# Kernel optimization log

Hardware: AMD Instinct MI355X
Metric: run time of the kernel (lower is better)

Reference implementation:

```python
import jax, jax.numpy as jnp
import numpy as np

N_NODES = 100000
N_EDGES = 1600000
D_IN = 64
D_HID = 64
NEG_SLOPE = 0.01  # torch leaky_relu default


def _sage_conv(x, src, dst, W_l, b_l, W_r):
    # PyG SAGEConv (mean aggr): lin_l(mean_j x_j) + lin_r(x_i)
    n = x.shape[0]
    msg = x[src]  # [E, D] irregular gather
    agg = jax.ops.segment_sum(msg, dst, num_segments=n)
    deg = jax.ops.segment_sum(jnp.ones((src.shape[0],), x.dtype), dst, num_segments=n)
    mean = agg / jnp.maximum(deg, 1.0)[:, None]
    return mean @ W_l.T + b_l + x @ W_r.T


def setup_inputs() -> dict:
    key = jax.random.key(0)
    ks = jax.random.split(key, 12)
    x = jax.random.normal(ks[0], (N_NODES, D_IN), dtype=jnp.float32)
    edge_index = jax.random.randint(ks[1], (2, N_EDGES), 0, N_NODES, dtype=jnp.int64)
    s = 1.0 / np.sqrt(D_IN)
    params = {}
    dims = [(D_IN, D_HID), (D_HID, D_HID), (D_HID, D_HID)]
    ki = 2
    for i, (din, dout) in enumerate(dims, start=1):
        sc = 1.0 / np.sqrt(din)
        params[f'W_l{i}'] = jax.random.uniform(ks[ki], (dout, din), minval=-sc, maxval=sc, dtype=jnp.float32); ki += 1
        params[f'b_l{i}'] = jnp.zeros((dout,), jnp.float32)
        params[f'W_r{i}'] = jax.random.uniform(ks[ki], (dout, din), minval=-sc, maxval=sc, dtype=jnp.float32); ki += 1
    sc = 1.0 / np.sqrt(D_HID)
    params['W_out'] = jax.random.uniform(ks[ki], (1, D_HID), minval=-sc, maxval=sc, dtype=jnp.float32)
    params['b_out'] = jnp.zeros((1,), jnp.float32)
    return {'x': x, 'edge_index': edge_index, **params}


def reference(x, edge_index, W_l1, b_l1, W_r1, W_l2, b_l2, W_r2, W_l3, b_l3, W_r3, W_out, b_out):
    src, dst = edge_index[0], edge_index[1]
    h = x
    for (Wl, bl, Wr) in ((W_l1, b_l1, W_r1), (W_l2, b_l2, W_r2), (W_l3, b_l3, W_r3)):
        h = _sage_conv(h, src, dst, Wl, bl, Wr)
        h = jnp.where(h >= 0, h, NEG_SLOPE * h)
        # dropout is identity in eval mode
    return h @ W_out.T + b_out  # [N, 1]
```

## Files before the change

### kernel.cpp

```cpp
#include <hip/hip_runtime.h>
#include <hip/hip_fp16.h>

#define D 64
#define NEG_SLOPE 0.01f
#define CB_SHIFT 9
#define CB_NODES 512
#define MAXCB 256
#define CHUNK 4096
#define BCAP 10240
#define SADJ_CAP 10240
#define SAH 72

typedef _Float16 f16x8 __attribute__((ext_vector_type(8)));
typedef _Float16 f16x4 __attribute__((ext_vector_type(4)));
typedef float    f32x4 __attribute__((ext_vector_type(4)));

struct GemmSmem {
    _Float16 sA[128 * SAH];
    _Float16 sW[2 * 64 * SAH];
};
struct ScatSmem {
    int hist[MAXCB];
    int lofs[MAXCB];
    int gbase[MAXCB];
    int cur[MAXCB];
    int swsum[4];
    unsigned spk[CHUNK];
    unsigned char sbk[CHUNK];
};
union FusedSmem { GemmSmem g; ScatSmem s; };

__device__ __forceinline__ int detect64(const void* __restrict__ ei) {
    int lane = threadIdx.x & 63;
    int v = ((const int*)ei)[2 * lane + 1];
    return (__ballot(v != 0) == 0ULL) ? 1 : 0;
}

__device__ __forceinline__ int edge_at(const void* __restrict__ ei, long long idx, int is64) {
    if (is64) return (int)((const long long*)ei)[idx];
    return ((const int*)ei)[idx];
}

__device__ __forceinline__ void scatter_body(ScatSmem& sm,
        const void* __restrict__ ei, long long E,
        int* __restrict__ bcursor, unsigned* __restrict__ ebuf,
        int ncb, int bid) {
    int t = threadIdx.x;
    sm.hist[t] = 0;
    int is64 = detect64(ei);
    __syncthreads();
    long long start = (long long)bid * CHUNK;
    int ccnt = (int)min((long long)CHUNK, E - start);

    for (int i = t; i < ccnt; i += 256) {
        int d = edge_at(ei, E + start + i, is64);
        atomicAdd(&sm.hist[d >> CB_SHIFT], 1);
    }
    __syncthreads();
    {
        int v = sm.hist[t];
        int lane = t & 63, w = t >> 6;
        int inc = v;
        for (int off = 1; off < 64; off <<= 1) {
            int u = __shfl_up(inc, off, 64);
            if (lane >= off) inc += u;
        }
        if (lane == 63) sm.swsum[w] = inc;
        __syncthreads();
        int wof = 0;
        for (int i = 0; i < w; ++i) wof += sm.swsum[i];
        sm.lofs[t] = wof + inc - v;
    }
    if (t < ncb && sm.hist[t]) sm.gbase[t] = atomicAdd(&bcursor[t], sm.hist[t]);
    __syncthreads();
    sm.cur[t] = sm.lofs[t];
    __syncthreads();

    for (int i = t; i < ccnt; i += 256) {
        int s = edge_at(ei, start + i, is64);
        int d = edge_at(ei, E + start + i, is64);
        int b = d >> CB_SHIFT;
        int slot = atomicAdd(&sm.cur[b], 1);
        sm.spk[slot] = ((unsigned)s << CB_SHIFT) | (unsigned)(d & (CB_NODES - 1));
        sm.sbk[slot] = (unsigned char)b;
    }
    __syncthreads();

    for (int i = t; i < ccnt; i += 256) {
        int b = sm.sbk[i];
        int dst = sm.gbase[b] + (i - sm.lofs[b]);
        if (dst < BCAP) ebuf[(size_t)b * BCAP + dst] = sm.spk[i];
    }
}

__device__ __forceinline__ void gemm_body(GemmSmem& sm,
        const float* __restrict__ h, const float* __restrict__ Wl,
        const float* __restrict__ Wr, const float* __restrict__ bl,
        __half* __restrict__ P, float* __restrict__ R, int N, int bid) {
    int t = threadIdx.x;
    int node_base = bid * 128;

    {
        int r = t >> 1, j = t & 1;
        int gn = node_base + r; if (gn >= N) gn = N - 1;
        const float* src = h + (size_t)gn * D + j * 32;
        _Float16* dst = sm.sA + r * SAH + j * 32;
#pragma unroll
        for (int q = 0; q < 8; ++q) {
            const float4 v = *(const float4*)(src + q * 4);
            f16x4 o = { (_Float16)v.x, (_Float16)v.y, (_Float16)v.z, (_Float16)v.w };
            *(f16x4*)(dst + q * 4) = o;
        }
    }
    {
        const float* W = (t < 128) ? Wl : Wr;
        int tt = t & 127;
        int r = tt >> 1, j = tt & 1;
        const float* src = W + r * D + j * 32;
        _Float16* dst = sm.sW + ((t < 128) ? 0 : 64 * SAH) + r * SAH + j * 32;
#pragma unroll
        for (int q = 0; q < 8; ++q) {
            const float4 v = *(const float4*)(src + q * 4);
            f16x4 o = { (_Float16)v.x, (_Float16)v.y, (_Float16)v.z, (_Float16)v.w };
            *(f16x4*)(dst + q * 4) = o;
        }
    }
    __syncthreads();

    int w = t >> 6, lane = t & 63;
    int lr = lane & 15;
    int lk = lane >> 4;

    f16x8 af[2][2];
#pragma unroll
    for (int mt = 0; mt < 2; ++mt)
#pragma unroll
        for (int ks = 0; ks < 2; ++ks)
            af[mt][ks] = *(const f16x8*)(sm.sA
                + (w * 32 + mt * 16 + lr) * SAH + ks * 32 + lk * 8);

    f32x4 accP[2][4], accR[2][4];
#pragma unroll
    for (int mt = 0; mt < 2; ++mt)
#pragma unroll
        for (int nt = 0; nt < 4; ++nt) {
            accP[mt][nt] = (f32x4){0.f, 0.f, 0.f, 0.f};
            accR[mt][nt] = (f32x4){0.f, 0.f, 0.f, 0.f};
        }

#pragma unroll
    for (int nt = 0; nt < 4; ++nt) {
        const _Float16* wrow = sm.sW + (nt * 16 + lr) * SAH + lk * 8;
        f16x8 b0 = *(const f16x8*)(wrow);
        f16x8 b1 = *(const f16x8*)(wrow + 32);
        f16x8 c0 = *(const f16x8*)(wrow + 64 * SAH);
        f16x8 c1 = *(const f16x8*)(wrow + 64 * SAH + 32);
        accP[0][nt] = __builtin_amdgcn_mfma_f32_16x16x32_f16(af[0][0], b0, accP[0][nt], 0, 0, 0);
        accP[0][nt] = __builtin_amdgcn_mfma_f32_16x16x32_f16(af[0][1], b1, accP[0][nt], 0, 0, 0);
        accP[1][nt] = __builtin_amdgcn_mfma_f32_16x16x32_f16(af[1][0], b0, accP[1][nt], 0, 0, 0);
        accP[1][nt] = __builtin_amdgcn_mfma_f32_16x16x32_f16(af[1][1], b1, accP[1][nt], 0, 0, 0);
        accR[0][nt] = __builtin_amdgcn_mfma_f32_16x16x32_f16(af[0][0], c0, accR[0][nt], 0, 0, 0);
        accR[0][nt] = __builtin_amdgcn_mfma_f32_16x16x32_f16(af[0][1], c1, accR[0][nt], 0, 0, 0);
        accR[1][nt] = __builtin_amdgcn_mfma_f32_16x16x32_f16(af[1][0], c0, accR[1][nt], 0, 0, 0);
        accR[1][nt] = __builtin_amdgcn_mfma_f32_16x16x32_f16(af[1][1], c1, accR[1][nt], 0, 0, 0);
    }

#pragma unroll
    for (int nt = 0; nt < 4; ++nt) {
        int ch = nt * 16 + lr;
        float bv = bl[ch];
#pragma unroll
        for (int mt = 0; mt < 2; ++mt) {
            int nrow = node_base + w * 32 + mt * 16 + lk * 4;
#pragma unroll
            for (int r = 0; r < 4; ++r) {
                int gn = nrow + r;
                if (gn < N) {
                    P[(size_t)gn * D + ch] = __float2half(accP[mt][nt][r]);
                    R[(size_t)gn * D + ch] = accR[mt][nt][r] + bv;
                }
            }
        }
    }
}

__global__ __launch_bounds__(256, 4) void gemm1_scatter_kernel(
        const void* __restrict__ ei, long long E,
        int* __restrict__ bcursor, unsigned* __restrict__ ebuf, int ncb, int sgrid,
        const float* __restrict__ h, const float* __restrict__ Wl,
        const float* __restrict__ Wr, const float* __restrict__ bl,
        __half* __restrict__ P, float* __restrict__ R, int N) {
    __shared__ FusedSmem sm;
    if ((int)blockIdx.x < sgrid) {
        scatter_body(sm.s, ei, E, bcursor, ebuf, ncb, blockIdx.x);
    } else {
        gemm_body(sm.g, h, Wl, Wr, bl, P, R, N, blockIdx.x - sgrid);
    }
}

__global__ __launch_bounds__(256, 4) void gemm_kernel(
        const float* __restrict__ h, const float* __restrict__ Wl,
        const float* __restrict__ Wr, const float* __restrict__ bl,
        __half* __restrict__ P, float* __restrict__ R, int N) {
    __shared__ GemmSmem sm;
    gemm_body(sm, h, Wl, Wr, bl, P, R, N, blockIdx.x);
}

__global__ __launch_bounds__(256) void finefill_kernel(
        const unsigned* __restrict__ ebuf, const int* __restrict__ bcount,
        int* __restrict__ rowptr, int* __restrict__ adj, int N, int ncb) {
    __shared__ int cnt[CB_NODES];
    __shared__ int cur[CB_NODES];
    __shared__ int wpart[4];
    __shared__ int wsum4[4];
    __shared__ int se0;
    __shared__ int sAdj[SADJ_CAP];
    int t = threadIdx.x;
    int b = blockIdx.x;

    {
        int v = (t < ncb) ? min(bcount[t], BCAP) : 0;
        int lane = t & 63, w = t >> 6;
        int inc = v;
        for (int off = 1; off < 64; off <<= 1) {
            int u = __shfl_up(inc, off, 64);
            if (lane >= off) inc += u;
        }
        if (lane == 63) wsum4[w] = inc;
        __syncthreads();
        int wof = 0;
        for (int iw = 0; iw < w; ++iw) wof += wsum4[iw];
        int ex = wof + inc - v;
        if (t == b) se0 = ex;
        if (b == 0 && t == 0)
            rowptr[N] = wsum4[0] + wsum4[1] + wsum4[2] + wsum4[3];
    }
    __syncthreads();
    int e0 = se0;
    int len = min(bcount[b], BCAP);
    int nb = b << CB_SHIFT;
    const unsigned* slab = ebuf + (size_t)b * BCAP;

    cnt[2 * t] = 0; cnt[2 * t + 1] = 0;
    __syncthreads();
    for (int i = t; i < len; i += 256) {
        unsigned p = slab[i];
        atomicAdd(&cnt[p & (CB_NODES - 1)], 1);
    }
    __syncthreads();

    int c0 = cnt[2 * t], c1 = cnt[2 * t + 1];
    int s = c0 + c1;
    int lane = t & 63, wv = t >> 6;
    int inc = s;
    for (int off = 1; off < 64; off <<= 1) {
        int u = __shfl_up(inc, off, 64);
        if (lane >= off) inc += u;
    }
    if (lane == 63) wpart[wv] = inc;
    __syncthreads();
    int wof = 0;
    for (int w = 0; w < wv; ++w) wof += wpart[w];
    int ex = wof + inc - s;
    cur[2 * t] = ex; cur[2 * t + 1] = ex + c0;
    {
        int g = nb + 2 * t;
        if (g < N)     rowptr[g]     = e0 + ex;
        if (g + 1 < N) rowptr[g + 1] = e0 + ex + c0;
    }
    __syncthreads();

    int big = (len > SADJ_CAP);
    for (int i = t; i < len; i += 256) {
        unsigned p = slab[i];
        int dl = (int)(p & (CB_NODES - 1));
        int src = (int)(p >> CB_SHIFT);
        int pos = atomicAdd(&cur[dl], 1);
        if (big) adj[e0 + pos] = src;
        else     sAdj[pos] = src;
    }
    __syncthreads();
    if (!big) {
        for (int i = t; i < len; i += 256) adj[e0 + i] = sAdj[i];
    }
}

__global__ __launch_bounds__(256) void agg3_kernel(
        const __half* __restrict__ P, const float* __restrict__ R,
        const int* __restrict__ rowptr, const int* __restrict__ adj,
        const float* __restrict__ Wout, const float* __restrict__ bout,
        float* __restrict__ hout, float* __restrict__ out,
        int N, int final_flag) {
    int tid = blockIdx.x * blockDim.x + threadIdx.x;
    int i = tid >> 3;
    int sub = tid & 7;
    if (i >= N) return;

    int b0 = rowptr[i], b1 = rowptr[i + 1];
    float a0 = 0.f, a1 = 0.f, a2 = 0.f, a3 = 0.f;
    float a4 = 0.f, a5 = 0.f, a6 = 0.f, a7 = 0.f;
    size_t cofs = (size_t)(sub << 3);

    int e = b0;
    int nfull = (b1 - b0) >> 2;
#pragma unroll 2
    for (int q = 0; q < nfull; ++q) {
        int s0 = adj[e], s1 = adj[e + 1], s2 = adj[e + 2], s3 = adj[e + 3];
        e += 4;
        union { float4 f4; __half2 h2[4]; } u0, u1, u2, u3;
        u0.f4 = *(const float4*)(P + (size_t)s0 * D + cofs);
        u1.f4 = *(const float4*)(P + (size_t)s1 * D + cofs);
        u2.f4 = *(const float4*)(P + (size_t)s2 * D + cofs);
        u3.f4 = *(const float4*)(P + (size_t)s3 * D + cofs);
#define ACC8(u) { \
        float2 v0 = __half22float2(u.h2[0]); float2 v1 = __half22float2(u.h2[1]); \
        float2 v2 = __half22float2(u.h2[2]); float2 v3 = __half22float2(u.h2[3]); \
        a0 += v0.x; a1 += v0.y; a2 += v1.x; a3 += v1.y; \
        a4 += v2.x; a5 += v2.y; a6 += v3.x; a7 += v3.y; }
        ACC8(u0) ACC8(u1) ACC8(u2) ACC8(u3)
    }
    for (; e < b1; ++e) {
        int s = adj[e];
        union { float4 f4; __half2 h2[4]; } u;
        u.f4 = *(const float4*)(P + (size_t)s * D + cofs);
        ACC8(u)
    }
#undef ACC8

    float inv = 1.0f / fmaxf((float)(b1 - b0), 1.0f);
    const float4 r0 = *(const float4*)(R + (size_t)i * D + cofs);
    const float4 r1 = *(const float4*)(R + (size_t)i * D + cofs + 4);
    float y0 = a0 * inv + r0.x; y0 = (y0 >= 0.f) ? y0 : NEG_SLOPE * y0;
    float y1 = a1 * inv + r0.y; y1 = (y1 >= 0.f) ? y1 : NEG_SLOPE * y1;
    float y2 = a2 * inv + r0.z; y2 = (y2 >= 0.f) ? y2 : NEG_SLOPE * y2;
    float y3 = a3 * inv + r0.w; y3 = (y3 >= 0.f) ? y3 : NEG_SLOPE * y3;
    float y4 = a4 * inv + r1.x; y4 = (y4 >= 0.f) ? y4 : NEG_SLOPE * y4;
    float y5 = a5 * inv + r1.y; y5 = (y5 >= 0.f) ? y5 : NEG_SLOPE * y5;
    float y6 = a6 * inv + r1.z; y6 = (y6 >= 0.f) ? y6 : NEG_SLOPE * y6;
    float y7 = a7 * inv + r1.w; y7 = (y7 >= 0.f) ? y7 : NEG_SLOPE * y7;
    if (!final_flag) {
        *(float4*)(hout + (size_t)i * D + cofs) = make_float4(y0, y1, y2, y3);
        *(float4*)(hout + (size_t)i * D + cofs + 4) = make_float4(y4, y5, y6, y7);
    } else {
        const float4 w0 = *(const float4*)(Wout + cofs);
        const float4 w1 = *(const float4*)(Wout + cofs + 4);
        float p = y0 * w0.x + y1 * w0.y + y2 * w0.z + y3 * w0.w
                + y4 * w1.x + y5 * w1.y + y6 * w1.z + y7 * w1.w;
        p += __shfl_xor(p, 1, 64);
        p += __shfl_xor(p, 2, 64);
        p += __shfl_xor(p, 4, 64);
        if (sub == 0) out[i] = p + bout[0];
    }
}

extern "C" void kernel_launch(void* const* d_in, const int* in_sizes, int n_in,
                              void* d_out, int out_size, void* d_ws, size_t ws_size,
                              hipStream_t stream) {
    const float* x    = (const float*)d_in[0];
    const void*  ei   = d_in[1];
    const float* Wl1  = (const float*)d_in[2];
    const float* bl1  = (const float*)d_in[3];
    const float* Wr1  = (const float*)d_in[4];
    const float* Wl2  = (const float*)d_in[5];
    const float* bl2  = (const float*)d_in[6];
    const float* Wr2  = (const float*)d_in[7];
    const float* Wl3  = (const float*)d_in[8];
    const float* bl3  = (const float*)d_in[9];
    const float* Wr3  = (const float*)d_in[10];
    const float* Wout = (const float*)d_in[11];
    const float* bout = (const float*)d_in[12];
    float* out = (float*)d_out;

    int       N = in_sizes[0] / D;
    long long E = (long long)in_sizes[1] / 2;
    int ncb = (N + CB_NODES - 1) >> CB_SHIFT;

    char* ws = (char*)d_ws;
    size_t off = 256;
    int* bcursor = (int*)(ws + off); off += 1024;
    int* rowptr = (int*)(ws + off); off += (((size_t)(N + 1) * 4 + 255) / 256) * 256;
    int* adj    = (int*)(ws + off); off += (((size_t)E * 4 + 255) / 256) * 256;
    unsigned* ebuf = (unsigned*)(ws + off); off += (size_t)ncb * BCAP * 4;
    float* B1 = (float*)(ws + off); off += (size_t)N * D * 4;
    __half* B2h = (__half*)(ws + off);

    int sgrid = (int)((E + CHUNK - 1) / CHUNK);
    int ggrid = (N + 127) / 128;
    int agrid = (N * 8 + 255) / 256;

    hipMemsetAsync(bcursor, 0, 1024, stream);

    gemm1_scatter_kernel<<<sgrid + ggrid, 256, 0, stream>>>(
        ei, E, bcursor, ebuf, ncb, sgrid,
        x, Wl1, Wr1, bl1, B2h, B1, N);
    finefill_kernel<<<ncb, 256, 0, stream>>>(ebuf, bcursor, rowptr, adj, N, ncb);
    agg3_kernel<<<agrid, 256, 0, stream>>>(B2h, B1, rowptr, adj, Wout, bout, B1, out, N, 0);
    gemm_kernel<<<ggrid, 256, 0, stream>>>(B1, Wl2, Wr2, bl2, B2h, B1, N);
    agg3_kernel<<<agrid, 256, 0, stream>>>(B2h, B1, rowptr, adj, Wout, bout, B1, out, N, 0);
    gemm_kernel<<<ggrid, 256, 0, stream>>>(B1, Wl3, Wr3, bl3, B2h, B1, N);
    agg3_kernel<<<agrid, 256, 0, stream>>>(B2h, B1, rowptr, adj, Wout, bout, B1, out, N, 1);
}
```

Before: 281.9 us.

## Switch to aggregate-then-transform with fp16 activations and a fused final projection

New measurement: 272.8 us. -3.2%, faster.

```diff
diff --git a/kernel.cpp b/kernel.cpp
--- a/kernel.cpp
+++ b/kernel.cpp
@@ -9,16 +9,11 @@
 #define CHUNK 4096
 #define BCAP 10240
 #define SADJ_CAP 10240
-#define SAH 72
+#define CGRID 256
 
 typedef _Float16 f16x8 __attribute__((ext_vector_type(8)));
-typedef _Float16 f16x4 __attribute__((ext_vector_type(4)));
 typedef float    f32x4 __attribute__((ext_vector_type(4)));
 
-struct GemmSmem {
-    _Float16 sA[128 * SAH];
-    _Float16 sW[2 * 64 * SAH];
-};
 struct ScatSmem {
     int hist[MAXCB];
     int lofs[MAXCB];
@@ -28,7 +23,6 @@
     unsigned spk[CHUNK];
     unsigned char sbk[CHUNK];
 };
-union FusedSmem { GemmSmem g; ScatSmem s; };
 
 __device__ __forceinline__ int detect64(const void* __restrict__ ei) {
     int lane = threadIdx.x & 63;
@@ -93,117 +87,138 @@
     }
 }
 
-__device__ __forceinline__ void gemm_body(GemmSmem& sm,
-        const float* __restrict__ h, const float* __restrict__ Wl,
-        const float* __restrict__ Wr, const float* __restrict__ bl,
-        __half* __restrict__ P, float* __restrict__ R, int N, int bid) {
+__device__ __forceinline__ void conv_body(const float* __restrict__ x,
+        _Float16* __restrict__ x16, long long U, int cid,
+        const float* __restrict__ Wl1, const float* __restrict__ Wr1,
+        const float* __restrict__ Wl2, const float* __restrict__ Wr2,
+        const float* __restrict__ Wl3, const float* __restrict__ Wr3,
+        _Float16* __restrict__ W16) {
     int t = threadIdx.x;
-    int node_base = bid * 128;
-
-    {
-        int r = t >> 1, j = t & 1;
-        int gn = node_base + r; if (gn >= N) gn = N - 1;
-        const float* src = h + (size_t)gn * D + j * 32;
-        _Float16* dst = sm.sA + r * SAH + j * 32;
-#pragma unroll
-        for (int q = 0; q < 8; ++q) {
-            const float4 v = *(const float4*)(src + q * 4);
-            f16x4 o = { (_Float16)v.x, (_Float16)v.y, (_Float16)v.z, (_Float16)v.w };
-            *(f16x4*)(dst + q * 4) = o;
+    for (long long u = (long long)cid * 256 + t; u < U; u += (long long)CGRID * 256) {
+        const float* s = x + u * 8;
+        const float4 v0 = *(const float4*)s;
+        const float4 v1 = *(const float4*)(s + 4);
+        f16x8 o = { (_Float16)v0.x, (_Float16)v0.y, (_Float16)v0.z, (_Float16)v0.w,
+                    (_Float16)v1.x, (_Float16)v1.y, (_Float16)v1.z, (_Float16)v1.w };
+        *(f16x8*)(x16 + u * 8) = o;
+    }
+    if (cid == 0) {
+        const float* Ws[6] = { Wl1, Wr1, Wl2, Wr2, Wl3, Wr3 };
+#pragma unroll
+        for (int m = 0; m < 6; ++m) {
+            const float* src = Ws[m];
+            _Float16* dst = W16 + m * 4096;
+            for (int i = t; i < 4096; i += 256) dst[i] = (_Float16)src[i];
         }
     }
-    {
-        const float* W = (t < 128) ? Wl : Wr;
-        int tt = t & 127;
-        int r = tt >> 1, j = tt & 1;
-        const float* src = W + r * D + j * 32;
-        _Float16* dst = sm.sW + ((t < 128) ? 0 : 64 * SAH) + r * SAH + j * 32;
-#pragma unroll
-        for (int q = 0; q < 8; ++q) {
-            const float4 v = *(const float4*)(src + q * 4);
-            f16x4 o = { (_Float16)v.x, (_Float16)v.y, (_Float16)v.z, (_Float16)v.w };
-            *(f16x4*)(dst + q * 4) = o;
-        }
-    }
-    __syncthreads();
-
-    int w = t >> 6, lane = t & 63;
+}
+
+__global__ __launch_bounds__(256, 6) void scatter_conv_kernel(
+        const void* __restrict__ ei, long long E,
+        int* __restrict__ bcursor, unsigned* __restrict__ ebuf, int ncb, int sgrid,
+        const float* __restrict__ x, _Float16* __restrict__ x16, long long U,
+        const float* __restrict__ Wl1, const float* __restrict__ Wr1,
+        const float* __restrict__ Wl2, const float* __restrict__ Wr2,
+        const float* __restrict__ Wl3, const float* __restrict__ Wr3,
+        _Float16* __restrict__ W16) {
+    __shared__ ScatSmem sm;
+    if ((int)blockIdx.x < sgrid)
+        scatter_body(sm, ei, E, bcursor, ebuf, ncb, blockIdx.x);
+    else
+        conv_body(x, x16, U, blockIdx.x - sgrid, Wl1, Wr1, Wl2, Wr2, Wl3, Wr3, W16);
+}
+
+__global__ __launch_bounds__(256) void sage_gemm_kernel(
+        const _Float16* __restrict__ Hin, const _Float16* __restrict__ MH,
+        const _Float16* __restrict__ W16,
+        const float* __restrict__ bl,
+        _Float16* __restrict__ Hout,
+        const float* __restrict__ Wout, const float* __restrict__ bout,
+        float* __restrict__ out, int N, int final_flag) {
+    int t = threadIdx.x, w = t >> 6, lane = t & 63;
     int lr = lane & 15;
     int lk = lane >> 4;
-
-    f16x8 af[2][2];
+    int rbase = (int)blockIdx.x * 128 + w * 32;
+
+    f16x8 ah[2][2], am[2][2];
+#pragma unroll
+    for (int mt = 0; mt < 2; ++mt) {
+        int gn = rbase + mt * 16 + lr;
+        if (gn >= N) gn = N - 1;
+        const _Float16* hp = Hin + (size_t)gn * D + lk * 8;
+        const _Float16* mp = MH  + (size_t)gn * D + lk * 8;
+        ah[mt][0] = *(const f16x8*)hp;  ah[mt][1] = *(const f16x8*)(hp + 32);
+        am[mt][0] = *(const f16x8*)mp;  am[mt][1] = *(const f16x8*)(mp + 32);
+    }
+
+    f32x4 acc[2][4];
 #pragma unroll
     for (int mt = 0; mt < 2; ++mt)
 #pragma unroll
-        for (int ks = 0; ks < 2; ++ks)
-            af[mt][ks] = *(const f16x8*)(sm.sA
-                + (w * 32 + mt * 16 + lr) * SAH + ks * 32 + lk * 8);
-
-    f32x4 accP[2][4], accR[2][4];
-#pragma unroll
-    for (int mt = 0; mt < 2; ++mt)
-#pragma unroll
-        for (int nt = 0; nt < 4; ++nt) {
-            accP[mt][nt] = (f32x4){0.f, 0.f, 0.f, 0.f};
-            accR[mt][nt] = (f32x4){0.f, 0.f, 0.f, 0.f};
-        }
-
+        for (int nt = 0; nt < 4; ++nt)
+            acc[mt][nt] = (f32x4){0.f, 0.f, 0.f, 0.f};
+
+    const _Float16* Wl = W16;
+    const _Float16* Wr = W16 + 4096;
 #pragma unroll
     for (int nt = 0; nt < 4; ++nt) {
-        const _Float16* wrow = sm.sW + (nt * 16 + lr) * SAH + lk * 8;
-        f16x8 b0 = *(const f16x8*)(wrow);
-        f16x8 b1 = *(const f16x8*)(wrow + 32);
-        f16x8 c0 = *(const f16x8*)(wrow + 64 * SAH);
-        f16x8 c1 = *(const f16x8*)(wrow + 64 * SAH + 32);
-        accP[0][nt] = __builtin_amdgcn_mfma_f32_16x16x32_f16(af[0][0], b0, accP[0][nt], 0, 0, 0);
-        accP[0][nt] = __builtin_amdgcn_mfma_f32_16x16x32_f16(af[0][1], b1, accP[0][nt], 0, 0, 0);
-        accP[1][nt] = __builtin_amdgcn_mfma_f32_16x16x32_f16(af[1][0], b0, accP[1][nt], 0, 0, 0);
-        accP[1][nt] = __builtin_amdgcn_mfma_f32_16x16x32_f16(af[1][1], b1, accP[1][nt], 0, 0, 0);
-        accR[0][nt] = __builtin_amdgcn_mfma_f32_16x16x32_f16(af[0][0], c0, accR[0][nt], 0, 0, 0);
-        accR[0][nt] = __builtin_amdgcn_mfma_f32_16x16x32_f16(af[0][1], c1, accR[0][nt], 0, 0, 0);
-        accR[1][nt] = __builtin_amdgcn_mfma_f32_16x16x32_f16(af[1][0], c0, accR[1][nt], 0, 0, 0);
-        accR[1][nt] = __builtin_amdgcn_mfma_f32_16x16x32_f16(af[1][1], c1, accR[1][nt], 0, 0, 0);
-    }
-
-#pragma unroll
-    for (int nt = 0; nt < 4; ++nt) {
-        int ch = nt * 16 + lr;
-        float bv = bl[ch];
-#pragma unroll
-        for (int mt = 0; mt < 2; ++mt) {
-            int nrow = node_base + w * 32 + mt * 16 + lk * 4;
+        const _Float16* pl = Wl + (nt * 16 + lr) * D + lk * 8;
+        const _Float16* pr = Wr + (nt * 16 + lr) * D + lk * 8;
+        f16x8 b0 = *(const f16x8*)pl;  f16x8 b1 = *(const f16x8*)(pl + 32);
+        f16x8 c0 = *(const f16x8*)pr;  f16x8 c1 = *(const f16x8*)(pr + 32);
+        acc[0][nt] = __builtin_amdgcn_mfma_f32_16x16x32_f16(am[0][0], b0, acc[0][nt], 0, 0, 0);
+        acc[0][nt] = __builtin_amdgcn_mfma_f32_16x16x32_f16(am[0][1], b1, acc[0][nt], 0, 0, 0);
+        acc[0][nt] = __builtin_amdgcn_mfma_f32_16x16x32_f16(ah[0][0], c0, acc[0][nt], 0, 0, 0);
+        acc[0][nt] = __builtin_amdgcn_mfma_f32_16x16x32_f16(ah[0][1], c1, acc[0][nt], 0, 0, 0);
+        acc[1][nt] = __builtin_amdgcn_mfma_f32_16x16x32_f16(am[1][0], b0, acc[1][nt], 0, 0, 0);
+        acc[1][nt] = __builtin_amdgcn_mfma_f32_16x16x32_f16(am[1][1], b1, acc[1][nt], 0, 0, 0);
+        acc[1][nt] = __builtin_amdgcn_mfma_f32_16x16x32_f16(ah[1][0], c0, acc[1][nt], 0, 0, 0);
+        acc[1][nt] = __builtin_amdgcn_mfma_f32_16x16x32_f16(ah[1][1], c1, acc[1][nt], 0, 0, 0);
+    }
+
+    float blv[4];
+#pragma unroll
+    for (int nt = 0; nt < 4; ++nt) blv[nt] = bl[nt * 16 + lr];
+
+    if (!final_flag) {
+#pragma unroll
+        for (int mt = 0; mt < 2; ++mt)
 #pragma unroll
             for (int r = 0; r < 4; ++r) {
-                int gn = nrow + r;
+                int gn = rbase + mt * 16 + lk * 4 + r;
                 if (gn < N) {
-                    P[(size_t)gn * D + ch] = __float2half(accP[mt][nt][r]);
-                    R[(size_t)gn * D + ch] = accR[mt][nt][r] + bv;
+#pragma unroll
+                    for (int nt = 0; nt < 4; ++nt) {
+                        float y = acc[mt][nt][r] + blv[nt];
+                        y = (y >= 0.f) ? y : NEG_SLOPE * y;
+                        Hout[(size_t)gn * D + nt * 16 + lr] = (_Float16)y;
+                    }
                 }
             }
-        }
-    }
-}
-
-__global__ __launch_bounds__(256, 4) void gemm1_scatter_kernel(
-        const void* __restrict__ ei, long long E,
-        int* __restrict__ bcursor, unsigned* __restrict__ ebuf, int ncb, int sgrid,
-        const float* __restrict__ h, const float* __restrict__ Wl,
-        const float* __restrict__ Wr, const float* __restrict__ bl,
-        __half* __restrict__ P, float* __restrict__ R, int N) {
-    __shared__ FusedSmem sm;
-    if ((int)blockIdx.x < sgrid) {
-        scatter_body(sm.s, ei, E, bcursor, ebuf, ncb, blockIdx.x);
     } else {
-        gemm_body(sm.g, h, Wl, Wr, bl, P, R, N, blockIdx.x - sgrid);
-    }
-}
-
-__global__ __launch_bounds__(256, 4) void gemm_kernel(
-        const float* __restrict__ h, const float* __restrict__ Wl,
-        const float* __restrict__ Wr, const float* __restrict__ bl,
-        __half* __restrict__ P, float* __restrict__ R, int N) {
-    __shared__ GemmSmem sm;
-    gemm_body(sm, h, Wl, Wr, bl, P, R, N, blockIdx.x);
+        float wv[4];
+#pragma unroll
+        for (int nt = 0; nt < 4; ++nt) wv[nt] = Wout[nt * 16 + lr];
+        float bo = bout[0];
+#pragma unroll
+        for (int mt = 0; mt < 2; ++mt)
+#pragma unroll
+            for (int r = 0; r < 4; ++r) {
+                float p = 0.f;
+#pragma unroll
+                for (int nt = 0; nt < 4; ++nt) {
+                    float y = acc[mt][nt][r] + blv[nt];
+                    y = (y >= 0.f) ? y : NEG_SLOPE * y;
+                    p += y * wv[nt];
+                }
+                p += __shfl_xor(p, 1, 64);
+                p += __shfl_xor(p, 2, 64);
+                p += __shfl_xor(p, 4, 64);
+                p += __shfl_xor(p, 8, 64);
+                int gn = rbase + mt * 16 + lk * 4 + r;
+                if (lr == 0 && gn < N) out[gn] = p + bo;
+            }
+    }
 }
 
 __global__ __launch_bounds__(256) void finefill_kernel(
@@ -285,12 +300,10 @@
     }
 }
 
-__global__ __launch_bounds__(256) void agg3_kernel(
-        const __half* __restrict__ P, const float* __restrict__ R,
+__global__ __launch_bounds__(256) void agg_kernel(
+        const _Float16* __restrict__ H,
         const int* __restrict__ rowptr, const int* __restrict__ adj,
-        const float* __restrict__ Wout, const float* __restrict__ bout,
-        float* __restrict__ hout, float* __restrict__ out,
-        int N, int final_flag) {
+        _Float16* __restrict__ MH, int N) {
     int tid = blockIdx.x * blockDim.x + threadIdx.x;
     int i = tid >> 3;
     int sub = tid & 7;
@@ -308,10 +321,10 @@
         int s0 = adj[e], s1 = adj[e + 1], s2 = adj[e + 2], s3 = adj[e + 3];
         e += 4;
         union { float4 f4; __half2 h2[4]; } u0, u1, u2, u3;
-        u0.f4 = *(const float4*)(P + (size_t)s0 * D + cofs);
-        u1.f4 = *(const float4*)(P + (size_t)s1 * D + cofs);
-        u2.f4 = *(const float4*)(P + (size_t)s2 * D + cofs);
-        u3.f4 = *(const float4*)(P + (size_t)s3 * D + cofs);
+        u0.f4 = *(const float4*)(H + (size_t)s0 * D + cofs);
+        u1.f4 = *(const float4*)(H + (size_t)s1 * D + cofs);
+        u2.f4 = *(const float4*)(H + (size_t)s2 * D + cofs);
+        u3.f4 = *(const float4*)(H + (size_t)s3 * D + cofs);
 #define ACC8(u) { \
         float2 v0 = __half22float2(u.h2[0]); float2 v1 = __half22float2(u.h2[1]); \
         float2 v2 = __half22float2(u.h2[2]); float2 v3 = __half22float2(u.h2[3]); \
@@ -322,35 +335,17 @@
     for (; e < b1; ++e) {
         int s = adj[e];
         union { float4 f4; __half2 h2[4]; } u;
-        u.f4 = *(const float4*)(P + (size_t)s * D + cofs);
+        u.f4 = *(const float4*)(H + (size_t)s * D + cofs);
         ACC8(u)
     }
 #undef ACC8
 
     float inv = 1.0f / fmaxf((float)(b1 - b0), 1.0f);
-    const float4 r0 = *(const float4*)(R + (size_t)i * D + cofs);
-    const float4 r1 = *(const float4*)(R + (size_t)i * D + cofs + 4);
-    float y0 = a0 * inv + r0.x; y0 = (y0 >= 0.f) ? y0 : NEG_SLOPE * y0;
-    float y1 = a1 * inv + r0.y; y1 = (y1 >= 0.f) ? y1 : NEG_SLOPE * y1;
-    float y2 = a2 * inv + r0.z; y2 = (y2 >= 0.f) ? y2 : NEG_SLOPE * y2;
-    float y3 = a3 * inv + r0.w; y3 = (y3 >= 0.f) ? y3 : NEG_SLOPE * y3;
-    float y4 = a4 * inv + r1.x; y4 = (y4 >= 0.f) ? y4 : NEG_SLOPE * y4;
-    float y5 = a5 * inv + r1.y; y5 = (y5 >= 0.f) ? y5 : NEG_SLOPE * y5;
-    float y6 = a6 * inv + r1.z; y6 = (y6 >= 0.f) ? y6 : NEG_SLOPE * y6;
-    float y7 = a7 * inv + r1.w; y7 = (y7 >= 0.f) ? y7 : NEG_SLOPE * y7;
-    if (!final_flag) {
-        *(float4*)(hout + (size_t)i * D + cofs) = make_float4(y0, y1, y2, y3);
-        *(float4*)(hout + (size_t)i * D + cofs + 4) = make_float4(y4, y5, y6, y7);
-    } else {
-        const float4 w0 = *(const float4*)(Wout + cofs);
-        const float4 w1 = *(const float4*)(Wout + cofs + 4);
-        float p = y0 * w0.x + y1 * w0.y + y2 * w0.z + y3 * w0.w
-                + y4 * w1.x + y5 * w1.y + y6 * w1.z + y7 * w1.w;
-        p += __shfl_xor(p, 1, 64);
-        p += __shfl_xor(p, 2, 64);
-        p += __shfl_xor(p, 4, 64);
-        if (sub == 0) out[i] = p + bout[0];
-    }
+    f16x8 o = { (_Float16)(a0 * inv), (_Float16)(a1 * inv),
+                (_Float16)(a2 * inv), (_Float16)(a3 * inv),
+                (_Float16)(a4 * inv), (_Float16)(a5 * inv),
+                (_Float16)(a6 * inv), (_Float16)(a7 * inv) };
+    *(f16x8*)(MH + (size_t)i * D + cofs) = o;
 }
 
 extern "C" void kernel_launch(void* const* d_in, const int* in_sizes, int n_in,
@@ -374,6 +369,7 @@
     int       N = in_sizes[0] / D;
     long long E = (long long)in_sizes[1] / 2;
     int ncb = (N + CB_NODES - 1) >> CB_SHIFT;
+    long long U = (long long)N * D / 8;
 
     char* ws = (char*)d_ws;
     size_t off = 256;
@@ -381,8 +377,11 @@
     int* rowptr = (int*)(ws + off); off += (((size_t)(N + 1) * 4 + 255) / 256) * 256;
     int* adj    = (int*)(ws + off); off += (((size_t)E * 4 + 255) / 256) * 256;
     unsigned* ebuf = (unsigned*)(ws + off); off += (size_t)ncb * BCAP * 4;
-    float* B1 = (float*)(ws + off); off += (size_t)N * D * 4;
-    __half* B2h = (__half*)(ws + off);
+    _Float16* x16 = (_Float16*)(ws + off); off += (size_t)N * D * 2;
+    _Float16* mh  = (_Float16*)(ws + off); off += (size_t)N * D * 2;
+    _Float16* hA  = (_Float16*)(ws + off); off += (size_t)N * D * 2;
+    _Float16* hB  = (_Float16*)(ws + off); off += (size_t)N * D * 2;
+    _Float16* W16 = (_Float16*)(ws + off); off += 6 * 4096 * 2;
 
     int sgrid = (int)((E + CHUNK - 1) / CHUNK);
     int ggrid = (N + 127) / 128;
@@ -390,13 +389,17 @@
 
     hipMemsetAsync(bcursor, 0, 1024, stream);
 
-    gemm1_scatter_kernel<<<sgrid + ggrid, 256, 0, stream>>>(
+    scatter_conv_kernel<<<sgrid + CGRID, 256, 0, stream>>>(
         ei, E, bcursor, ebuf, ncb, sgrid,
-        x, Wl1, Wr1, bl1, B2h, B1, N);
+        x, x16, U, Wl1, Wr1, Wl2, Wr2, Wl3, Wr3, W16);
     finefill_kernel<<<ncb, 256, 0, stream>>>(ebuf, bcursor, rowptr, adj, N, ncb);
-    agg3_kernel<<<agrid, 256, 0, stream>>>(B2h, B1, rowptr, adj, Wout, bout, B1, out, N, 0);
-    gemm_kernel<<<ggrid, 256, 0, stream>>>(B1, Wl2, Wr2, bl2, B2h, B1, N);
-    agg3_kernel<<<agrid, 256, 0, stream>>>(B2h, B1, rowptr, adj, Wout, bout, B1, out, N, 0);
-    gemm_kernel<<<ggrid, 256, 0, stream>>>(B1, Wl3, Wr3, bl3, B2h, B1, N);
-    agg3_kernel<<<agrid, 256, 0, stream>>>(B2h, B1, rowptr, adj, Wout, bout, B1, out, N, 1);
-}
+    agg_kernel<<<agrid, 256, 0, stream>>>(x16, rowptr, adj, mh, N);
+    sage_gemm_kernel<<<ggrid, 256, 0, stream>>>(x16, mh, W16, bl1, hA,
+                                                Wout, bout, out, N, 0);
+    agg_kernel<<<agrid, 256, 0, stream>>>(hA, rowptr, adj, mh, N);
+    sage_gemm_kernel<<<ggrid, 256, 0, stream>>>(hA, mh, W16 + 2 * 4096, bl2, hB,
+                                                Wout, bout, out, N, 0);
+    agg_kernel<<<agrid, 256, 0, stream>>>(hB, rowptr, adj, mh, N);
+    sage_gemm_kernel<<<ggrid, 256, 0, stream>>>(hB, mh, W16 + 4 * 4096, bl3, hA,
+                                                Wout, bout, out, N, 1);
+}
```
